# Optimization experiments

Hardware: AMD Instinct MI355X
Metric: run time of the kernel (lower is better)

## Reference

```python
import jax, jax.numpy as jnp
import numpy as np

N = 65536      # total nodes
B = 512        # graphs (equal-sized)
NPER = N // B  # 128 nodes per graph
E = 655360     # edges
F_IN = 128
K = 32         # sort-pool k
OUT = 27


def _gcn(x, row, col, dinv, W, b):
    # PyG GCNConv with added self-loops and symmetric normalization:
    xw = x @ W                                   # [N, F_out]
    coef = dinv[row] * dinv[col]                 # [E]
    agg = jax.ops.segment_sum(xw[row] * coef[:, None], col, num_segments=N)
    return agg + (dinv * dinv)[:, None] * xw + b  # self-loop term + bias


def _conv1d(x, w, b, stride):
    # x: [B, C_in, L], w: [C_out, C_in, K]
    out = jax.lax.conv_general_dilated(x, w, (stride,), 'VALID',
                                       dimension_numbers=('NCH', 'OIH', 'NCH'))
    return out + b[None, :, None]


def setup_inputs() -> dict:
    key = jax.random.key(0)
    ks = jax.random.split(key, 16)
    x = jax.random.normal(ks[0], (N, F_IN), dtype=jnp.float32)
    edge_index = jax.random.randint(ks[1], (2, E), 0, N, dtype=jnp.int32)
    batch = jnp.repeat(jnp.arange(B, dtype=jnp.int32), NPER)

    def lin(k, fi, fo):
        return jax.random.normal(k, (fi, fo), dtype=jnp.float32) / np.sqrt(fi)

    W1, b1 = lin(ks[2], F_IN, 128), jnp.zeros((128,), jnp.float32)
    W2, b2 = lin(ks[3], 128, 64), jnp.zeros((64,), jnp.float32)
    W3, b3 = lin(ks[4], 64, 32), jnp.zeros((32,), jnp.float32)
    W4, b4 = lin(ks[5], 32, 32), jnp.zeros((32,), jnp.float32)
    conv5_w = jax.random.normal(ks[6], (16, 1, 256), jnp.float32) / np.sqrt(256)
    conv5_b = jnp.zeros((16,), jnp.float32)
    conv6_w = jax.random.normal(ks[7], (32, 16, 5), jnp.float32) / np.sqrt(16 * 5)
    conv6_b = jnp.zeros((32,), jnp.float32)
    dense_w = lin(ks[8], 384, OUT)
    dense_b = jnp.zeros((OUT,), jnp.float32)
    return dict(x=x, edge_index=edge_index, batch=batch,
                W1=W1, b1=b1, W2=W2, b2=b2, W3=W3, b3=b3, W4=W4, b4=b4,
                conv5_w=conv5_w, conv5_b=conv5_b, conv6_w=conv6_w, conv6_b=conv6_b,
                dense_w=dense_w, dense_b=dense_b)


def reference(x, edge_index, batch, W1, b1, W2, b2, W3, b3, W4, b4,
              conv5_w, conv5_b, conv6_w, conv6_b, dense_w, dense_b):
    row, col = edge_index[0], edge_index[1]
    deg = jax.ops.segment_sum(jnp.ones((E,), x.dtype), col, num_segments=N) + 1.0
    dinv = jax.lax.rsqrt(deg)

    x1 = jnp.tanh(_gcn(x, row, col, dinv, W1, b1))
    x2 = jnp.tanh(_gcn(x1, row, col, dinv, W2, b2))
    x3 = jnp.tanh(_gcn(x2, row, col, dinv, W3, b3))
    x4 = jnp.tanh(_gcn(x3, row, col, dinv, W4, b4))
    h = jnp.concatenate([x1, x2, x3, x4], axis=-1)   # [N, 256]

    # SortAggregation: sort nodes within each graph by last channel (desc), take top-k.
    hg = h.reshape(B, NPER, 256)
    idx = jnp.argsort(-hg[:, :, -1], axis=1)[:, :K]                 # [B, K]
    pooled = jnp.take_along_axis(hg, idx[:, :, None], axis=1)       # [B, K, 256]
    top_k_indices = idx + (jnp.arange(B, dtype=idx.dtype) * NPER)[:, None]

    z = pooled.reshape(B, 1, K * 256)                # [B, 1, 8192]
    z = jax.nn.relu(_conv1d(z, conv5_w, conv5_b, 256))  # [B, 16, 32]
    z = jax.lax.reduce_window(z, -jnp.inf, jax.lax.max,
                              (1, 1, 2), (1, 1, 2), 'VALID')        # [B, 16, 16]
    z = jax.nn.relu(_conv1d(z, conv6_w, conv6_b, 1))  # [B, 32, 12]
    z = z.reshape(B, -1)                              # [B, 384]
    out = z @ dense_w + dense_b                       # [B, 27]
    return out, top_k_indices
```

## Files before the change

kernel.cpp:

```cpp
#include <hip/hip_runtime.h>
#include <math.h>

#define N_NODES 65536
#define N_EDGES 655360
#define N_GRAPHS 512
#define NPERG 128
#define KTOP 32
#define NOUT 27
#define OUT0_SIZE (N_GRAPHS * NOUT)
#define EPS 64

typedef unsigned int uint32;
typedef unsigned short u16;
typedef unsigned char u8;
typedef __attribute__((ext_vector_type(8))) short bf16x8;
typedef __attribute__((ext_vector_type(4))) float f32x4;
typedef __attribute__((ext_vector_type(2))) float f32x2;

__device__ __forceinline__ float blo(uint32 u) { return __uint_as_float(u << 16); }
__device__ __forceinline__ float bhi(uint32 u) { return __uint_as_float(u & 0xffff0000u); }
__device__ __forceinline__ u16 f2b(float f) {
    uint32 u = __float_as_uint(f);
    u += 0x7fffu + ((u >> 16) & 1u);
    return (u16)(u >> 16);
}
__device__ __forceinline__ uint32 pk(float a, float b) {
    return (uint32)f2b(a) | ((uint32)f2b(b) << 16);
}
__device__ __forceinline__ f32x2 fp8lo(uint32 u) { return __builtin_amdgcn_cvt_pk_f32_fp8((int)u, false); }
__device__ __forceinline__ f32x2 fp8hi(uint32 u) { return __builtin_amdgcn_cvt_pk_f32_fp8((int)u, true); }
__device__ __forceinline__ u8 f2fp8(float v) {
    return (u8)(__builtin_amdgcn_cvt_pk_fp8_f32(v, v, 0, false) & 0xff);
}


__global__ __launch_bounds__(256) void zero_kernel(int* __restrict__ cur) {
    cur[blockIdx.x * 256 + threadIdx.x] = 0;
}


template<int FI, int FO>
__device__ __forceinline__ void pack_w(const float* __restrict__ W, uint4* __restrict__ pw,
                                       int base, int nb) {
    constexpr int KC = FI / 8;
    for (int q = (blockIdx.x - base) * 256 + threadIdx.x; q < FO * KC; q += nb * 256) {
        int n = q % FO, c = q / FO;
        const float* wp = W + (size_t)(c * 8) * FO + n;
        uint4 v;
        v.x = pk(wp[0],            wp[(size_t)FO]);
        v.y = pk(wp[2*(size_t)FO], wp[3*(size_t)FO]);
        v.z = pk(wp[4*(size_t)FO], wp[5*(size_t)FO]);
        v.w = pk(wp[6*(size_t)FO], wp[7*(size_t)FO]);
        pw[n * KC + c] = v;
    }
}

__global__ __launch_bounds__(256) void prep_w(const float* __restrict__ W1, const float* __restrict__ W2,
                                              const float* __restrict__ W3, const float* __restrict__ W4,
                                              uint4* __restrict__ pw1, uint4* __restrict__ pw2,
                                              uint4* __restrict__ pw3, uint4* __restrict__ pw4) {
    int b = blockIdx.x;
    if (b < 8)       pack_w<128, 128>(W1, pw1, 0, 8);
    else if (b < 12) pack_w<128, 64>(W2, pw2, 8, 4);
    else if (b < 13) pack_w<64, 32>(W3, pw3, 12, 1);
    else             pack_w<32, 32>(W4, pw4, 13, 1);
}


__global__ __launch_bounds__(256) void fill_kernel(const int* __restrict__ erow, const int* __restrict__ ecol,
                                                   int* __restrict__ cur, u16* __restrict__ ep) {
    int e = blockIdx.x * 256 + threadIdx.x;
    int r = erow[e], d = ecol[e];
    int slot = atomicAdd(&cur[d], 1);
    if (slot < EPS) ep[(d << 6) + slot] = (u16)r;
}


__global__ __launch_bounds__(256) void dinv_kernel(const int* __restrict__ cur, float* __restrict__ dinv) {
    int i = blockIdx.x * 256 + threadIdx.x;
    dinv[i] = rsqrtf((float)cur[i] + 1.0f);
}


template<int FI, int FO>
__device__ __forceinline__ void stage_Bp(const uint4* __restrict__ pw, uint4* __restrict__ Bs) {
    constexpr int KC = FI / 8, SA = KC + 1;
    for (int q = threadIdx.x; q < FO * KC; q += 256) {
        int n = q / KC, c = q % KC;
        Bs[n * SA + c] = pw[q];
    }
}

template<int FI, int FO, bool OUT_FP8>
__device__ __forceinline__ void mfma_store(uint4* __restrict__ As, const uint4* __restrict__ Bs,
                                           uint4* __restrict__ Y, size_t rowbase,
                                           const float* __restrict__ ds) {
    constexpr int KC = FI / 8, SA = KC + 1;
    constexpr int NTILE = FO / 16;
    constexpr int CW = (NTILE >= 4) ? 4 : NTILE;
    constexpr int NTW = NTILE / CW;
    constexpr int RW = 4 / CW;
    constexpr int RS = 2 / RW;
    constexpr int KSTEPS = FI / 32;
    int t = threadIdx.x;
    int w = t >> 6, L = t & 63;
    int quad = L >> 4, m = L & 15;
    int cw = w % CW, rw = w / CW;

    const bf16x8* Asv = (const bf16x8*)As;
    const bf16x8* Bsv = (const bf16x8*)Bs;

    f32x4 acc[RS][NTW];
#pragma unroll
    for (int i = 0; i < RS; i++)
#pragma unroll
        for (int j = 0; j < NTW; j++) acc[i][j] = (f32x4)0.f;

#pragma unroll
    for (int ks = 0; ks < KSTEPS; ks++) {
        int kc = ks * 4 + quad;
        bf16x8 bfr[NTW];
#pragma unroll
        for (int j = 0; j < NTW; j++) {
            int n = (cw * NTW + j) * 16 + m;
            bfr[j] = Bsv[n * SA + kc];
        }
#pragma unroll
        for (int i = 0; i < RS; i++) {
            int r = (rw * RS + i) * 16 + m;
            bf16x8 afr = Asv[r * SA + kc];
#pragma unroll
            for (int j = 0; j < NTW; j++)
                acc[i][j] = __builtin_amdgcn_mfma_f32_16x16x32_bf16(afr, bfr[j], acc[i][j], 0, 0, 0);
        }
    }
    __syncthreads();

    if constexpr (OUT_FP8) {
        u8* outs = (u8*)As;
#pragma unroll
        for (int i = 0; i < RS; i++) {
            int rb = (rw * RS + i) * 16 + quad * 4;
#pragma unroll
            for (int j = 0; j < NTW; j++) {
                int cc = (cw * NTW + j) * 16 + m;
#pragma unroll
                for (int g2 = 0; g2 < 4; g2++)
                    outs[(rb + g2) * FO + cc] = f2fp8(acc[i][j][g2] * ds[rb + g2]);
            }
        }
    } else {
        u16* outs = (u16*)As;
#pragma unroll
        for (int i = 0; i < RS; i++) {
            int rb = (rw * RS + i) * 16 + quad * 4;
#pragma unroll
            for (int j = 0; j < NTW; j++) {
                int cc = (cw * NTW + j) * 16 + m;
#pragma unroll
                for (int g2 = 0; g2 < 4; g2++)
                    outs[(rb + g2) * FO + cc] = f2b(acc[i][j][g2] * ds[rb + g2]);
            }
        }
    }
    __syncthreads();
    constexpr int NU4 = OUT_FP8 ? (32 * FO / 16) : (32 * FO / 8);
    for (int q = t; q < NU4; q += 256)
        Y[rowbase * (NU4 / 32) + q] = ((const uint4*)As)[q];
}


__global__ __launch_bounds__(256) void gemm1_kernel(const float* __restrict__ x,
                                                    const uint4* __restrict__ pw1,
                                                    const float* __restrict__ dinv,
                                                    uint4* __restrict__ xw1) {
    constexpr int KC = 16, SA = 17;
    __shared__ __align__(16) uint4 As[32 * SA];
    __shared__ __align__(16) uint4 Bs[128 * SA];
    __shared__ float ds[32];
    int t = threadIdx.x;
    stage_Bp<128, 128>(pw1, Bs);
    size_t rowbase = (size_t)blockIdx.x * 32;
    if (t < 32) ds[t] = dinv[rowbase + t];
    for (int q = t; q < 32 * KC; q += 256) {
        int r = q / KC, c = q % KC;
        const float* xp = x + (rowbase + r) * 128 + c * 8;
        float4 v0 = *(const float4*)xp;
        float4 v1 = *(const float4*)(xp + 4);
        uint4 u;
        u.x = pk(v0.x, v0.y); u.y = pk(v0.z, v0.w);
        u.z = pk(v1.x, v1.y); u.w = pk(v1.z, v1.w);
        As[r * SA + c] = u;
    }
    __syncthreads();
    mfma_store<128, 128, true>(As, Bs, xw1, rowbase, ds);
}


template<int F>
__device__ __forceinline__ void gath8_fp8v(const uint2* __restrict__ x2, uint4 e8,
                                           int cl, int rem, float (&ac)[8]) {
    constexpr int LN = F / 8;
    uint32 qq[8] = { e8.x & 0xffffu, e8.x >> 16, e8.y & 0xffffu, e8.y >> 16,
                     e8.z & 0xffffu, e8.z >> 16, e8.w & 0xffffu, e8.w >> 16 };
#pragma unroll
    for (int j = 0; j < 8; j++) {
        bool ok = j < rem;
        uint32 src = ok ? qq[j] : 0u;
        uint2 g = x2[(size_t)src * LN + cl];
        uint32 gx = ok ? g.x : 0u, gy = ok ? g.y : 0u;
        f32x2 l0 = fp8lo(gx), h0 = fp8hi(gx), l1 = fp8lo(gy), h1 = fp8hi(gy);
        ac[0] += l0.x; ac[1] += l0.y; ac[2] += h0.x; ac[3] += h0.y;
        ac[4] += l1.x; ac[5] += l1.y; ac[6] += h1.x; ac[7] += h1.y;
    }
}

template<int F>
__device__ __forceinline__ void agg_node_fp8v(const uint2* __restrict__ x2,
                                              const u16* __restrict__ ep,
                                              int n, int cl, int deg, float dn,
                                              const float* __restrict__ bias, float (&r)[8]) {
    constexpr int LN = F / 8;
    const u16* epp = ep + (n << 6);
    float ac[8];
#pragma unroll
    for (int c = 0; c < 8; c++) ac[c] = 0.f;
    uint4 e0 = *(const uint4*)(epp);
    uint4 e1 = *(const uint4*)(epp + 8);
    gath8_fp8v<F>(x2, e0, cl, deg, ac);
    gath8_fp8v<F>(x2, e1, cl, deg - 8, ac);
    if (deg > 16) {
        int nb = min((deg + 7) >> 3, EPS / 8);
        for (int b = 2; b < nb; b++) {
            uint4 e8 = *(const uint4*)(epp + b * 8);
            gath8_fp8v<F>(x2, e8, cl, deg - b * 8, ac);
        }
    }
    uint2 sv = x2[(size_t)n * LN + cl];
    f32x2 l0 = fp8lo(sv.x), h0 = fp8hi(sv.x), l1 = fp8lo(sv.y), h1 = fp8hi(sv.y);
    float sf[8] = { l0.x, l0.y, h0.x, h0.y, l1.x, l1.y, h1.x, h1.y };
#pragma unroll
    for (int c = 0; c < 8; c++) r[c] = dn * (ac[c] + sf[c]) + bias[8 * cl + c];
}


template<int F, int FO, bool OUT_FP8>
__global__ __launch_bounds__(256, 6) void agg_gemm8(const uint2* __restrict__ xin,
                                                    const int* __restrict__ cur,
                                                    const u16* __restrict__ ep,
                                                    const float* __restrict__ dinv,
                                                    const float* __restrict__ bias,
                                                    const uint4* __restrict__ pw,
                                                    uint4* __restrict__ hc4, int co4,
                                                    uint4* __restrict__ xout) {
    constexpr int KC = F / 8, SA = KC + 1;
    constexpr int LN = F / 8;
    constexpr int NPP = 256 / LN;
    __shared__ __align__(16) uint4 As[32 * SA];
    __shared__ __align__(16) uint4 Bs[FO * SA];
    __shared__ float ds[32];
    int t = threadIdx.x;
    int rowbase = blockIdx.x * 32;
    stage_Bp<F, FO>(pw, Bs);
    if (t < 32) ds[t] = dinv[rowbase + t];
    __syncthreads();

    int cl = t % LN, nsub = t / LN;
#pragma unroll
    for (int pass = 0; pass < 32 / NPP; pass++) {
        int nl = pass * NPP + nsub;
        int n = rowbase + nl;
        int deg = cur[n];
        float r[8];
        agg_node_fp8v<F>(xin, ep, n, cl, deg, ds[nl], bias, r);
        uint4 pr;
        pr.x = pk(tanhf(r[0]), tanhf(r[1]));
        pr.y = pk(tanhf(r[2]), tanhf(r[3]));
        pr.z = pk(tanhf(r[4]), tanhf(r[5]));
        pr.w = pk(tanhf(r[6]), tanhf(r[7]));
        hc4[(size_t)n * 32 + co4 + cl] = pr;
        As[nl * SA + cl] = pr;
    }
    __syncthreads();
    mfma_store<F, FO, OUT_FP8>(As, Bs, xout, (size_t)rowbase, ds);
}


template<int L4>
__device__ __forceinline__ void gath8_bf16(const uint2* __restrict__ x2, uint4 e8,
                                           int c4, int rem, float (&ac)[4][4]) {
    uint32 qq[8] = { e8.x & 0xffffu, e8.x >> 16, e8.y & 0xffffu, e8.y >> 16,
                     e8.z & 0xffffu, e8.z >> 16, e8.w & 0xffffu, e8.w >> 16 };
#pragma unroll
    for (int j = 0; j < 8; j++) {
        bool ok = j < rem;
        uint32 src = ok ? qq[j] : 0u;
        uint2 g = x2[(size_t)src * L4 + c4];
        uint32 gx = ok ? g.x : 0u, gy = ok ? g.y : 0u;
        ac[j & 3][0] += blo(gx); ac[j & 3][1] += bhi(gx);
        ac[j & 3][2] += blo(gy); ac[j & 3][3] += bhi(gy);
    }
}

template<int F>
__device__ __forceinline__ void agg_node_bf16(const uint2* __restrict__ x2,
                                              const u16* __restrict__ ep,
                                              int n, int c4, int deg, float dn,
                                              const float* __restrict__ bias,
                                              float& r0, float& r1, float& r2, float& r3) {
    constexpr int L4 = F / 4;
    const u16* epp = ep + (n << 6);
    float ac[4][4];
#pragma unroll
    for (int i = 0; i < 4; i++)
#pragma unroll
        for (int j = 0; j < 4; j++) ac[i][j] = 0.f;
    uint4 e0 = *(const uint4*)(epp);
    uint4 e1 = *(const uint4*)(epp + 8);
    gath8_bf16<L4>(x2, e0, c4, deg, ac);
    gath8_bf16<L4>(x2, e1, c4, deg - 8, ac);
    if (deg > 16) {
        int nb = min((deg + 7) >> 3, EPS / 8);
        for (int b = 2; b < nb; b++) {
            uint4 e8 = *(const uint4*)(epp + b * 8);
            gath8_bf16<L4>(x2, e8, c4, deg - b * 8, ac);
        }
    }
    float s0 = (ac[0][0] + ac[1][0]) + (ac[2][0] + ac[3][0]);
    float s1 = (ac[0][1] + ac[1][1]) + (ac[2][1] + ac[3][1]);
    float s2 = (ac[0][2] + ac[1][2]) + (ac[2][2] + ac[3][2]);
    float s3 = (ac[0][3] + ac[1][3]) + (ac[2][3] + ac[3][3]);
    uint2 sv = x2[(size_t)n * L4 + c4];
    r0 = dn * (s0 + blo(sv.x)) + bias[4 * c4 + 0];
    r1 = dn * (s1 + bhi(sv.x)) + bias[4 * c4 + 1];
    r2 = dn * (s2 + blo(sv.y)) + bias[4 * c4 + 2];
    r3 = dn * (s3 + bhi(sv.y)) + bias[4 * c4 + 3];
}


template<int F, int FO>
__global__ __launch_bounds__(256, 6) void agg_gemm_bf(const uint32* __restrict__ xin,
                                                      const int* __restrict__ cur,
                                                      const u16* __restrict__ ep,
                                                      const float* __restrict__ dinv,
                                                      const float* __restrict__ bias,
                                                      const uint4* __restrict__ pw,
                                                      uint32* __restrict__ hc, int co2,
                                                      uint4* __restrict__ xout) {
    constexpr int KC = F / 8, SA = KC + 1;
    constexpr int L4 = F / 4;
    constexpr int NPP = 256 / L4;
    __shared__ __align__(16) uint4 As[32 * SA];
    __shared__ __align__(16) uint4 Bs[FO * SA];
    __shared__ float ds[32];
    int t = threadIdx.x;
    int rowbase = blockIdx.x * 32;
    stage_Bp<F, FO>(pw, Bs);
    if (t < 32) ds[t] = dinv[rowbase + t];
    __syncthreads();

    uint2* As2 = (uint2*)As;
    uint2* hc2 = (uint2*)hc;
    int c4 = t % L4;
    int nsub = t / L4;
#pragma unroll
    for (int pass = 0; pass < 32 / NPP; pass++) {
        int nl = pass * NPP + nsub;
        int n = rowbase + nl;
        int deg = cur[n];
        float r0, r1, r2, r3;
        agg_node_bf16<F>((const uint2*)xin, ep, n, c4, deg, ds[nl], bias, r0, r1, r2, r3);
        uint2 pr;
        pr.x = pk(tanhf(r0), tanhf(r1));
        pr.y = pk(tanhf(r2), tanhf(r3));
        hc2[(size_t)n * 64 + co2 + c4] = pr;
        As2[nl * (SA * 2) + c4] = pr;
    }
    __syncthreads();
    mfma_store<F, FO, false>(As, Bs, xout, (size_t)rowbase, ds);
}


__global__ __launch_bounds__(256) void agg_last(const uint32* __restrict__ xin,
                                                const int* __restrict__ cur,
                                                const u16* __restrict__ ep,
                                                const float* __restrict__ dinv,
                                                const float* __restrict__ b4,
                                                uint32* __restrict__ hc) {
    int t = threadIdx.x;
    int c4 = t & 7, nsub = t >> 3;
    int n = blockIdx.x * 32 + nsub;
    int deg = cur[n];
    float dn = dinv[n];
    float r0, r1, r2, r3;
    agg_node_bf16<32>((const uint2*)xin, ep, n, c4, deg, dn, b4, r0, r1, r2, r3);
    uint2 pr;
    pr.x = pk(tanhf(r0), tanhf(r1));
    pr.y = pk(tanhf(r2), tanhf(r3));
    ((uint2*)hc)[(size_t)n * 64 + 56 + c4] = pr;
}


__global__ __launch_bounds__(256) void final_kernel(const uint32* __restrict__ hc,
                                                    const float* __restrict__ w5, const float* __restrict__ b5,
                                                    const float* __restrict__ w6, const float* __restrict__ b6,
                                                    const float* __restrict__ dw, const float* __restrict__ db,
                                                    float* __restrict__ out) {
    __shared__ float skey[128];
    __shared__ int   sidx[128];
    __shared__ uint32 ph[32 * 133];
    __shared__ float w5s[4096];
    __shared__ float z5[16 * 33];
    __shared__ float ms[16 * 17];
    __shared__ float z6[384];
    int g = blockIdx.x, t = threadIdx.x;

    for (int q = t; q < 4096; q += 256) w5s[q] = w5[q];
    if (t < 128) { skey[t] = bhi(hc[(size_t)(g * NPERG + t) * 128 + 127]); sidx[t] = t; }
    __syncthreads();

    for (int sz = 2; sz <= 128; sz <<= 1) {
        for (int stride = sz >> 1; stride > 0; stride >>= 1) {
            if (t < 64) {
                int i = ((t & ~(stride - 1)) << 1) | (t & (stride - 1));
                int j = i | stride;
                float ki = skey[i], kj = skey[j];
                int ii = sidx[i], ij = sidx[j];
                bool desc = ((i & sz) == 0);
                bool ibef = (ki > kj) || (ki == kj && ii < ij);
                if (desc != ibef) { skey[i] = kj; skey[j] = ki; sidx[i] = ij; sidx[j] = ii; }
            }
            __syncthreads();
        }
    }

    if (t < KTOP) out[OUT0_SIZE + g * KTOP + t] = (float)(g * NPERG + sidx[t]);

    {
        const uint4* hcv = (const uint4*)hc;
        int rsub = t >> 5, cell = t & 31;
#pragma unroll
        for (int p = 0; p < 4; p++) {
            int r2 = p * 8 + rsub;
            int node = g * NPERG + sidx[r2];
            uint4 v = hcv[(size_t)node * 32 + cell];
            uint32* dst = &ph[r2 * 133 + cell * 4];
            dst[0] = v.x; dst[1] = v.y; dst[2] = v.z; dst[3] = v.w;
        }
    }
    __syncthreads();

    {
        int o = t >> 5, l = t & 31;
        float a0 = 0.f, a1 = 0.f;
#pragma unroll 4
        for (int j2 = 0; j2 < 128; j2++) {
            uint32 u = ph[l * 133 + j2];
            float p0 = blo(u), p1 = bhi(u);
            a0 += p0 * w5s[o * 256 + 2 * j2]       + p1 * w5s[o * 256 + 2 * j2 + 1];
            a1 += p0 * w5s[(o + 8) * 256 + 2 * j2] + p1 * w5s[(o + 8) * 256 + 2 * j2 + 1];
        }
        z5[o * 33 + l]       = fmaxf(a0 + b5[o], 0.f);
        z5[(o + 8) * 33 + l] = fmaxf(a1 + b5[o + 8], 0.f);
    }
    __syncthreads();

    {
        int o = t >> 4, p = t & 15;
        ms[o * 17 + p] = fmaxf(z5[o * 33 + 2 * p], z5[o * 33 + 2 * p + 1]);
    }
    __syncthreads();

    for (int q = t; q < 384; q += 256) {
        int o2 = q / 12, tt = q % 12;
        float a = b6[o2];
        for (int o = 0; o < 16; o++) {
#pragma unroll
            for (int k = 0; k < 5; k++)
                a += w6[(o2 * 16 + o) * 5 + k] * ms[o * 17 + tt + k];
        }
        z6[q] = fmaxf(a, 0.f);
    }
    __syncthreads();

    if (t < NOUT) {
        float a = db[t];
        for (int i = 0; i < 384; i++) a += z6[i] * dw[i * NOUT + t];
        out[g * NOUT + t] = a;
    }
}


extern "C" void kernel_launch(void* const* d_in, const int* in_sizes, int n_in,
                              void* d_out, int out_size, void* d_ws, size_t ws_size,
                              hipStream_t stream) {
    const float* x    = (const float*)d_in[0];
    const int*   edge = (const int*)d_in[1];
    const int*   erow = edge;
    const int*   ecol = edge + N_EDGES;
    const float* W1 = (const float*)d_in[3];  const float* b1 = (const float*)d_in[4];
    const float* W2 = (const float*)d_in[5];  const float* b2 = (const float*)d_in[6];
    const float* W3 = (const float*)d_in[7];  const float* b3 = (const float*)d_in[8];
    const float* W4 = (const float*)d_in[9];  const float* b4 = (const float*)d_in[10];
    const float* w5 = (const float*)d_in[11]; const float* b5 = (const float*)d_in[12];
    const float* w6 = (const float*)d_in[13]; const float* b6 = (const float*)d_in[14];
    const float* dw = (const float*)d_in[15]; const float* db = (const float*)d_in[16];
    float* out = (float*)d_out;

    char* wsb = (char*)d_ws;
    size_t off = 0;
    auto alloc = [&](size_t bytes) -> void* {
        void* p = wsb + off;
        off = (off + bytes + 255) & ~(size_t)255;
        return p;
    };
    int*    cur  = (int*)   alloc((size_t)N_NODES * 4);
    float*  dinv = (float*) alloc((size_t)N_NODES * 4);
    u16*    ep   = (u16*)   alloc((size_t)N_NODES * EPS * 2);
    uint32* xwA  = (uint32*)alloc((size_t)N_NODES * 32 * 4);
    uint32* xwB  = (uint32*)alloc((size_t)N_NODES * 32 * 4);
    uint32* hc   = (uint32*)alloc((size_t)N_NODES * 128 * 4);
    uint4*  pw1  = (uint4*) alloc(2048 * 16);
    uint4*  pw2  = (uint4*) alloc(1024 * 16);
    uint4*  pw3  = (uint4*) alloc(256 * 16);
    uint4*  pw4  = (uint4*) alloc(128 * 16);
    (void)ws_size; (void)in_sizes; (void)n_in; (void)out_size;

    zero_kernel<<<N_NODES / 256, 256, 0, stream>>>(cur);
    prep_w<<<14, 256, 0, stream>>>(W1, W2, W3, W4, pw1, pw2, pw3, pw4);
    fill_kernel<<<N_EDGES / 256, 256, 0, stream>>>(erow, ecol, cur, ep);
    dinv_kernel<<<N_NODES / 256, 256, 0, stream>>>(cur, dinv);
    gemm1_kernel<<<N_NODES / 32, 256, 0, stream>>>(x, pw1, dinv, (uint4*)xwA);
    agg_gemm8<128, 64, true><<<N_NODES / 32, 256, 0, stream>>>((const uint2*)xwA, cur, ep, dinv, b1, pw2, (uint4*)hc, 0, (uint4*)xwB);
    agg_gemm8<64, 32, false><<<N_NODES / 32, 256, 0, stream>>>((const uint2*)xwB, cur, ep, dinv, b2, pw3, (uint4*)hc, 16, (uint4*)xwA);
    agg_gemm_bf<32, 32><<<N_NODES / 32, 256, 0, stream>>>(xwA, cur, ep, dinv, b3, pw4, hc, 48, (uint4*)xwB);
    agg_last<<<N_NODES / 32, 256, 0, stream>>>(xwB, cur, ep, dinv, b4, hc);
    final_kernel<<<N_GRAPHS, 256, 0, stream>>>(hc, w5, b5, w6, b6, dw, db, out);
}
```

Measured before the change: 232.0 us.

## Fuse last GCN layer into sort-pool kernel, computing only needed nodes

Removes the zero, dinv and agg_last kernels. The zeroing of cur moves into the weight-prep kernel, and dinv is recomputed inline from the degree counts. The final kernel now computes the sort key (the last channel of layer 4) for all 128 nodes per graph with a single-channel gather. It then runs the full layer-4 aggregation only for the 32 selected top-k nodes, which avoids computing layer 4 for the 96 discarded nodes per graph. The cost is extra gather work inside the per-graph kernel, done by only 128 threads with serial degree loops.

Result: faster. 226.1 us (median of 2 runs) (-2.5%).

```diff
diff --git a/kernel.cpp b/kernel.cpp
--- a/kernel.cpp
+++ b/kernel.cpp
@@ -31,11 +31,6 @@
 __device__ __forceinline__ f32x2 fp8hi(uint32 u) { return __builtin_amdgcn_cvt_pk_f32_fp8((int)u, true); }
 __device__ __forceinline__ u8 f2fp8(float v) {
     return (u8)(__builtin_amdgcn_cvt_pk_fp8_f32(v, v, 0, false) & 0xff);
-}
-
-
-__global__ __launch_bounds__(256) void zero_kernel(int* __restrict__ cur) {
-    cur[blockIdx.x * 256 + threadIdx.x] = 0;
 }
 
 
@@ -55,15 +50,18 @@
     }
 }
 
-__global__ __launch_bounds__(256) void prep_w(const float* __restrict__ W1, const float* __restrict__ W2,
-                                              const float* __restrict__ W3, const float* __restrict__ W4,
-                                              uint4* __restrict__ pw1, uint4* __restrict__ pw2,
-                                              uint4* __restrict__ pw3, uint4* __restrict__ pw4) {
+__global__ __launch_bounds__(256) void prep_kernel(const float* __restrict__ W1, const float* __restrict__ W2,
+                                                   const float* __restrict__ W3, const float* __restrict__ W4,
+                                                   uint4* __restrict__ pw1, uint4* __restrict__ pw2,
+                                                   uint4* __restrict__ pw3, uint4* __restrict__ pw4,
+                                                   int* __restrict__ cur) {
     int b = blockIdx.x;
-    if (b < 8)       pack_w<128, 128>(W1, pw1, 0, 8);
-    else if (b < 12) pack_w<128, 64>(W2, pw2, 8, 4);
-    else if (b < 13) pack_w<64, 32>(W3, pw3, 12, 1);
-    else             pack_w<32, 32>(W4, pw4, 13, 1);
+    if (b < 256) { cur[b * 256 + threadIdx.x] = 0; return; }
+    b -= 256;
+    if (b < 8)       pack_w<128, 128>(W1, pw1, 256, 8);
+    else if (b < 12) pack_w<128, 64>(W2, pw2, 264, 4);
+    else if (b < 13) pack_w<64, 32>(W3, pw3, 268, 1);
+    else             pack_w<32, 32>(W4, pw4, 269, 1);
 }
 
 
@@ -73,12 +71,6 @@
     int r = erow[e], d = ecol[e];
     int slot = atomicAdd(&cur[d], 1);
     if (slot < EPS) ep[(d << 6) + slot] = (u16)r;
-}
-
-
-__global__ __launch_bounds__(256) void dinv_kernel(const int* __restrict__ cur, float* __restrict__ dinv) {
-    int i = blockIdx.x * 256 + threadIdx.x;
-    dinv[i] = rsqrtf((float)cur[i] + 1.0f);
 }
 
 
@@ -172,7 +164,7 @@
 
 __global__ __launch_bounds__(256) void gemm1_kernel(const float* __restrict__ x,
                                                     const uint4* __restrict__ pw1,
-                                                    const float* __restrict__ dinv,
+                                                    const int* __restrict__ cur,
                                                     uint4* __restrict__ xw1) {
     constexpr int KC = 16, SA = 17;
     __shared__ __align__(16) uint4 As[32 * SA];
@@ -181,7 +173,7 @@
     int t = threadIdx.x;
     stage_Bp<128, 128>(pw1, Bs);
     size_t rowbase = (size_t)blockIdx.x * 32;
-    if (t < 32) ds[t] = dinv[rowbase + t];
+    if (t < 32) ds[t] = rsqrtf((float)cur[rowbase + t] + 1.0f);
     for (int q = t; q < 32 * KC; q += 256) {
         int r = q / KC, c = q % KC;
         const float* xp = x + (rowbase + r) * 128 + c * 8;
@@ -248,7 +240,6 @@
 __global__ __launch_bounds__(256, 6) void agg_gemm8(const uint2* __restrict__ xin,
                                                     const int* __restrict__ cur,
                                                     const u16* __restrict__ ep,
-                                                    const float* __restrict__ dinv,
                                                     const float* __restrict__ bias,
                                                     const uint4* __restrict__ pw,
                                                     uint4* __restrict__ hc4, int co4,
@@ -262,7 +253,7 @@
     int t = threadIdx.x;
     int rowbase = blockIdx.x * 32;
     stage_Bp<F, FO>(pw, Bs);
-    if (t < 32) ds[t] = dinv[rowbase + t];
+    if (t < 32) ds[t] = rsqrtf((float)cur[rowbase + t] + 1.0f);
     __syncthreads();
 
     int cl = t % LN, nsub = t / LN;
@@ -342,7 +333,6 @@
 __global__ __launch_bounds__(256, 6) void agg_gemm_bf(const uint32* __restrict__ xin,
                                                       const int* __restrict__ cur,
                                                       const u16* __restrict__ ep,
-                                                      const float* __restrict__ dinv,
                                                       const float* __restrict__ bias,
                                                       const uint4* __restrict__ pw,
                                                       uint32* __restrict__ hc, int co2,
@@ -356,7 +346,7 @@
     int t = threadIdx.x;
     int rowbase = blockIdx.x * 32;
     stage_Bp<F, FO>(pw, Bs);
-    if (t < 32) ds[t] = dinv[rowbase + t];
+    if (t < 32) ds[t] = rsqrtf((float)cur[rowbase + t] + 1.0f);
     __syncthreads();
 
     uint2* As2 = (uint2*)As;
@@ -381,27 +371,24 @@
 }
 
 
-__global__ __launch_bounds__(256) void agg_last(const uint32* __restrict__ xin,
-                                                const int* __restrict__ cur,
-                                                const u16* __restrict__ ep,
-                                                const float* __restrict__ dinv,
-                                                const float* __restrict__ b4,
-                                                uint32* __restrict__ hc) {
-    int t = threadIdx.x;
-    int c4 = t & 7, nsub = t >> 3;
-    int n = blockIdx.x * 32 + nsub;
-    int deg = cur[n];
-    float dn = dinv[n];
-    float r0, r1, r2, r3;
-    agg_node_bf16<32>((const uint2*)xin, ep, n, c4, deg, dn, b4, r0, r1, r2, r3);
-    uint2 pr;
-    pr.x = pk(tanhf(r0), tanhf(r1));
-    pr.y = pk(tanhf(r2), tanhf(r3));
-    ((uint2*)hc)[(size_t)n * 64 + 56 + c4] = pr;
-}
-
+__device__ __forceinline__ void key_g8(const uint32* __restrict__ xw, uint4 e8,
+                                       int rem, float (&ac3)[4]) {
+    uint32 qq[8] = { e8.x & 0xffffu, e8.x >> 16, e8.y & 0xffffu, e8.y >> 16,
+                     e8.z & 0xffffu, e8.z >> 16, e8.w & 0xffffu, e8.w >> 16 };
+#pragma unroll
+    for (int j = 0; j < 8; j++) {
+        bool ok = j < rem;
+        uint32 src = ok ? qq[j] : 0u;
+        uint32 gy = xw[(size_t)src * 16 + 15];
+        ac3[j & 3] += bhi(ok ? gy : 0u);
+    }
+}
 
 __global__ __launch_bounds__(256) void final_kernel(const uint32* __restrict__ hc,
+                                                    const uint32* __restrict__ xw4,
+                                                    const int* __restrict__ cur,
+                                                    const u16* __restrict__ ep,
+                                                    const float* __restrict__ b4,
                                                     const float* __restrict__ w5, const float* __restrict__ b5,
                                                     const float* __restrict__ w6, const float* __restrict__ b6,
                                                     const float* __restrict__ dw, const float* __restrict__ db,
@@ -409,14 +396,38 @@
     __shared__ float skey[128];
     __shared__ int   sidx[128];
     __shared__ uint32 ph[32 * 133];
-    __shared__ float w5s[4096];
+    __shared__ __align__(16) float w5s[4096];
     __shared__ float z5[16 * 33];
     __shared__ float ms[16 * 17];
     __shared__ float z6[384];
     int g = blockIdx.x, t = threadIdx.x;
 
-    for (int q = t; q < 4096; q += 256) w5s[q] = w5[q];
-    if (t < 128) { skey[t] = bhi(hc[(size_t)(g * NPERG + t) * 128 + 127]); sidx[t] = t; }
+    if (t >= 128) {
+        for (int q = t - 128; q < 1024; q += 128)
+            ((float4*)w5s)[q] = ((const float4*)w5)[q];
+    } else {
+        int n = g * NPERG + t;
+        int deg = cur[n];
+        float dn = rsqrtf((float)deg + 1.0f);
+        const u16* epp = ep + (n << 6);
+        float ac3[4] = { 0.f, 0.f, 0.f, 0.f };
+        uint4 e0 = *(const uint4*)(epp);
+        uint4 e1 = *(const uint4*)(epp + 8);
+        key_g8(xw4, e0, deg, ac3);
+        key_g8(xw4, e1, deg - 8, ac3);
+        if (deg > 16) {
+            int nb = min((deg + 7) >> 3, EPS / 8);
+            for (int b = 2; b < nb; b++) {
+                uint4 e8 = *(const uint4*)(epp + b * 8);
+                key_g8(xw4, e8, deg - b * 8, ac3);
+            }
+        }
+        float s3 = (ac3[0] + ac3[1]) + (ac3[2] + ac3[3]);
+        uint32 svy = xw4[(size_t)n * 16 + 15];
+        float r3 = dn * (s3 + bhi(svy)) + b4[31];
+        skey[t] = __uint_as_float(((uint32)f2b(tanhf(r3))) << 16);
+        sidx[t] = t;
+    }
     __syncthreads();
 
     for (int sz = 2; sz <= 128; sz <<= 1) {
@@ -437,11 +448,23 @@
     if (t < KTOP) out[OUT0_SIZE + g * KTOP + t] = (float)(g * NPERG + sidx[t]);
 
     {
+        int r = t >> 3, c4 = t & 7;
+        int n = g * NPERG + sidx[r];
+        int deg = cur[n];
+        float dn = rsqrtf((float)deg + 1.0f);
+        float r0, r1, r2, r3;
+        agg_node_bf16<32>((const uint2*)xw4, ep, n, c4, deg, dn, b4, r0, r1, r2, r3);
+        uint32* dst = &ph[r * 133 + 112 + 2 * c4];
+        dst[0] = pk(tanhf(r0), tanhf(r1));
+        dst[1] = pk(tanhf(r2), tanhf(r3));
+    }
+
+    {
         const uint4* hcv = (const uint4*)hc;
-        int rsub = t >> 5, cell = t & 31;
-#pragma unroll
-        for (int p = 0; p < 4; p++) {
-            int r2 = p * 8 + rsub;
+        for (int q = t; q < 1024; q += 256) {
+            int cell = q & 31;
+            if (cell >= 28) continue;
+            int r2 = q >> 5;
             int node = g * NPERG + sidx[r2];
             uint4 v = hcv[(size_t)node * 32 + cell];
             uint32* dst = &ph[r2 * 133 + cell * 4];
@@ -515,7 +538,6 @@
         return p;
     };
     int*    cur  = (int*)   alloc((size_t)N_NODES * 4);
-    float*  dinv = (float*) alloc((size_t)N_NODES * 4);
     u16*    ep   = (u16*)   alloc((size_t)N_NODES * EPS * 2);
     uint32* xwA  = (uint32*)alloc((size_t)N_NODES * 32 * 4);
     uint32* xwB  = (uint32*)alloc((size_t)N_NODES * 32 * 4);
@@ -526,14 +548,11 @@
     uint4*  pw4  = (uint4*) alloc(128 * 16);
     (void)ws_size; (void)in_sizes; (void)n_in; (void)out_size;
 
-    zero_kernel<<<N_NODES / 256, 256, 0, stream>>>(cur);
-    prep_w<<<14, 256, 0, stream>>>(W1, W2, W3, W4, pw1, pw2, pw3, pw4);
+    prep_kernel<<<270, 256, 0, stream>>>(W1, W2, W3, W4, pw1, pw2, pw3, pw4, cur);
     fill_kernel<<<N_EDGES / 256, 256, 0, stream>>>(erow, ecol, cur, ep);
-    dinv_kernel<<<N_NODES / 256, 256, 0, stream>>>(cur, dinv);
-    gemm1_kernel<<<N_NODES / 32, 256, 0, stream>>>(x, pw1, dinv, (uint4*)xwA);
-    agg_gemm8<128, 64, true><<<N_NODES / 32, 256, 0, stream>>>((const uint2*)xwA, cur, ep, dinv, b1, pw2, (uint4*)hc, 0, (uint4*)xwB);
-    agg_gemm8<64, 32, false><<<N_NODES / 32, 256, 0, stream>>>((const uint2*)xwB, cur, ep, dinv, b2, pw3, (uint4*)hc, 16, (uint4*)xwA);
-    agg_gemm_bf<32, 32><<<N_NODES / 32, 256, 0, stream>>>(xwA, cur, ep, dinv, b3, pw4, hc, 48, (uint4*)xwB);
-    agg_last<<<N_NODES / 32, 256, 0, stream>>>(xwB, cur, ep, dinv, b4, hc);
-    final_kernel<<<N_GRAPHS, 256, 0, stream>>>(hc, w5, b5, w6, b6, dw, db, out);
-}
+    gemm1_kernel<<<N_NODES / 32, 256, 0, stream>>>(x, pw1, cur, (uint4*)xwA);
+    agg_gemm8<128, 64, true><<<N_NODES / 32, 256, 0, stream>>>((const uint2*)xwA, cur, ep, b1, pw2, (uint4*)hc, 0, (uint4*)xwB);
+    agg_gemm8<64, 32, false><<<N_NODES / 32, 256, 0, stream>>>((const uint2*)xwB, cur, ep, b2, pw3, (uint4*)hc, 16, (uint4*)xwA);
+    agg_gemm_bf<32, 32><<<N_NODES / 32, 256, 0, stream>>>(xwA, cur, ep, b3, pw4, hc, 48, (uint4*)xwB);
+    final_kernel<<<N_GRAPHS, 256, 0, stream>>>(hc, xwB, cur, ep, b4, w5, b5, w6, b6, dw, db, out);
+}
```
